# Kernel tuning notes

Measured on AMD Instinct MI355X. Metric: run time of the kernel, lower is better.

Reference implementation:

```python
import jax, jax.numpy as jnp
import numpy as np

B, D_BYTES, R, S, NSEG, OUT_DIM = 8, 128, 4096, 32768, 1024, 512
D_BITS = 8 * D_BYTES  # 1024


def setup_inputs() -> dict:
    key = jax.random.key(0)
    ks = jax.random.split(key, 9)
    u8 = lambda k, shape: jax.random.randint(k, shape, 0, 256, dtype=jnp.int32).astype(jnp.uint8)
    Q = u8(ks[0], (B, D_BYTES))
    Q_ok = u8(ks[1], (B, D_BYTES))
    refs = u8(ks[2], (R, D_BYTES))
    ok_pos = u8(ks[3], (R, D_BYTES))
    ref2seg = jax.random.randint(ks[4], (S,), 0, R, dtype=jnp.int32)
    segments = jnp.sort(jax.random.randint(ks[5], (S,), 0, NSEG, dtype=jnp.int32))
    W_o = jax.random.normal(ks[6], (D_BITS, OUT_DIM), dtype=jnp.float32) * (1.0 / np.sqrt(D_BITS))
    b_o = jnp.zeros((OUT_DIM,), dtype=jnp.float32)
    return {"Q": Q, "Q_ok": Q_ok, "refs": refs, "ok_pos": ok_pos,
            "ref2seg": ref2seg, "segments": segments, "N": NSEG,
            "W_o": W_o, "b_o": b_o}


def reference(Q, Q_ok, refs, ok_pos, ref2seg, segments, N, W_o, b_o):
    # values: unpack packed reference bit-sequences once: (R, d_bits) uint8
    values = jnp.unpackbits(refs, axis=1)

    def per_query(q, q_ok):
        # popcount sequence similarity, normalized by non-gap overlap length
        ok = jnp.sum(jax.lax.population_count(jnp.bitwise_and(q_ok, ok_pos)), axis=1)      # (R,)
        match = jnp.sum(jax.lax.population_count(jnp.bitwise_and(q, refs)), axis=1)        # (R,)
        dists = match / ok                                                                  # (R,) float32
        # numerically-stable segment softmax over ragged neighborhoods
        applied = jnp.take(dists, ref2seg)                                                  # (S,)
        mx = jnp.take(jax.ops.segment_max(applied, segments, num_segments=N), segments)
        e = applied - mx
        norm = jnp.take(jnp.log(jax.ops.segment_sum(jnp.exp(e), segments, num_segments=N)), segments)
        scores = jnp.exp(e - norm)                                                          # (S,)
        # gather values along edges, weight, scatter-sum into segments
        av = jnp.take(values, ref2seg, axis=0) * scores[:, None]                            # (S, d_bits)
        return jax.ops.segment_sum(av, segments, num_segments=N)                            # (N, d_bits)

    V = jax.vmap(per_query)(Q, Q_ok)        # (B, N, d_bits)
    return V @ W_o + b_o                     # (B, N, out_dim)
```

## Files before the change

kernel.cpp:

```cpp
#include <hip/hip_runtime.h>

#define B_Q   8
#define DB    128
#define R_REF 4096
#define S_EDGE 32768
#define NSEG  1024
#define DBITS 1024
#define OUTD  512

#define NB_WCONV 128
#define NB_UNPACK 2048
#define NB_DIST 8192
#define TILE_E 256

typedef __bf16 bf16_t;
typedef bf16_t bf16x8 __attribute__((ext_vector_type(8)));
typedef float  f32x4  __attribute__((ext_vector_type(4)));
typedef unsigned int u32;

__device__ inline unsigned short f2bf(float f){
  unsigned int u = __builtin_bit_cast(unsigned int, f);
  u = (u + 0x7fffu + ((u >> 16) & 1u)) >> 16;
  return (unsigned short)u;
}

__device__ __forceinline__ void gl_lds16(const unsigned short* g, unsigned short* l){
  __builtin_amdgcn_global_load_lds((const __attribute__((address_space(1))) u32*)g,
                                   (__attribute__((address_space(3))) u32*)l, 16, 0, 0);
}

__global__ __launch_bounds__(256) void k_prep(const float* __restrict__ W,
                                              unsigned short* __restrict__ WT,
                                              const int* __restrict__ refs,
                                              unsigned short* __restrict__ Rb,
                                              const int* __restrict__ Q,
                                              const int* __restrict__ Qok,
                                              const int* __restrict__ okpos,
                                              float* __restrict__ distsT){
  __shared__ float tile[64][65];
  const int bid = blockIdx.x;
  const int tid = threadIdx.x;

  if (bid < NB_WCONV){
    const int k0 = (bid & 15) * 64, o0 = (bid >> 4) * 64;
    const int tr = tid >> 6, tc = tid & 63;
    #pragma unroll
    for (int i = 0; i < 16; ++i)
      tile[tr + i*4][tc] = W[(size_t)(k0 + tr + i*4) * OUTD + o0 + tc];
    __syncthreads();
    #pragma unroll
    for (int i = 0; i < 16; ++i)
      WT[(size_t)(o0 + tr + i*4) * DBITS + k0 + tc] = f2bf(tile[tc][tr + i*4]);
  } else if (bid < NB_WCONV + NB_UNPACK){
    int t = (bid - NB_WCONV) * 256 + tid;
    int row = t >> 7, byte = t & 127;
    u32 v = (u32)refs[row * DB + byte];
    uint4 o;
    u32* w = (u32*)&o;
    #pragma unroll
    for (int i2 = 0; i2 < 4; ++i2){
      u32 b0 = (v >> (7 - 2*i2)) & 1u;
      u32 b1 = (v >> (6 - 2*i2)) & 1u;
      w[i2] = b0 * 0x3F80u | ((b1 * 0x3F80u) << 16);
    }
    *(uint4*)(Rb + (size_t)row * DBITS + byte * 8) = o;
  } else {
    int pair = (bid - NB_WCONV - NB_UNPACK) * 4 + (tid >> 6);
    int l = tid & 63;
    int b = pair >> 12;
    int r = pair & 4095;
    int q0 = Q[b*DB + l],    q1 = Q[b*DB + 64 + l];
    int a0 = Qok[b*DB + l],  a1 = Qok[b*DB + 64 + l];
    int f0 = refs[r*DB + l], f1 = refs[r*DB + 64 + l];
    int p0 = okpos[r*DB + l],p1 = okpos[r*DB + 64 + l];
    int m = __popc(q0 & f0) + __popc(q1 & f1);
    int o = __popc(a0 & p0) + __popc(a1 & p1);
    int v = m | (o << 16);
    #pragma unroll
    for (int off = 32; off; off >>= 1) v += __shfl_down(v, off);
    if (l == 0) distsT[r * 8 + b] = (float)(v & 0xffff) / (float)(v >> 16);
  }
}

__global__ __launch_bounds__(256) void k_ugemm(const unsigned short* __restrict__ Rb,
                                               const unsigned short* __restrict__ WT,
                                               unsigned short* __restrict__ U){
  __shared__ unsigned short As[2][64 * 128];
  __shared__ unsigned short Bs[2][64 * 128];
  const int tid = threadIdx.x;
  const int w = tid >> 6, l = tid & 63;
  const int tm = blockIdx.x * 64, tn = blockIdx.y * 64;
  const int wm = (w & 1) * 32, wn = (w >> 1) * 32;
  const int lr = l & 15, kq = l >> 4;

  f32x4 acc[2][2] = {};
  int cur = 0;

  #define STAGE(buf, K0)                                                                   \
    do {                                                                                   \
      _Pragma("unroll")                                                                    \
      for (int c = 0; c < 4; ++c){                                                         \
        int idx = c * 256 + tid;                                                           \
        int row = idx >> 4, ch = idx & 15;                                                 \
        int gch = ch ^ (row & 15);                                                         \
        gl_lds16(Rb + (size_t)(tm + row) * DBITS + (K0) + gch*8,                           \
                 As[buf] + row*128 + ch*8);                                                \
        gl_lds16(WT + (size_t)(tn + row) * DBITS + (K0) + gch*8,                           \
                 Bs[buf] + row*128 + ch*8);                                                \
      }                                                                                    \
    } while (0)

  STAGE(0, 0);
  __syncthreads();

  for (int s = 0; s < 8; ++s){
    if (s < 7) STAGE(cur ^ 1, (s + 1) * 128);
    #pragma unroll
    for (int kk = 0; kk < 4; ++kk){
      bf16x8 af[2], bfr[2];
      #pragma unroll
      for (int m = 0; m < 2; ++m){
        int row = wm + m*16 + lr;
        int ch  = (kk*4 + kq) ^ (row & 15);
        af[m] = __builtin_bit_cast(bf16x8, *(const uint4*)(As[cur] + row*128 + ch*8));
      }
      #pragma unroll
      for (int n = 0; n < 2; ++n){
        int row = wn + n*16 + lr;
        int ch  = (kk*4 + kq) ^ (row & 15);
        bfr[n] = __builtin_bit_cast(bf16x8, *(const uint4*)(Bs[cur] + row*128 + ch*8));
      }
      #pragma unroll
      for (int m = 0; m < 2; ++m)
        #pragma unroll
        for (int n = 0; n < 2; ++n)
          acc[m][n] = __builtin_amdgcn_mfma_f32_16x16x32_bf16(af[m], bfr[n], acc[m][n], 0, 0, 0);
    }
    __syncthreads();
    cur ^= 1;
  }
  #undef STAGE

  #pragma unroll
  for (int n = 0; n < 2; ++n)
    #pragma unroll
    for (int m = 0; m < 2; ++m){
      int row = tm + wm + m*16 + kq*4;
      int col = tn + wn + n*16 + lr;
      #pragma unroll
      for (int q = 0; q < 4; ++q)
        U[(size_t)(row + q) * OUTD + col] = f2bf(acc[m][n][q]);
    }
}

__global__ __launch_bounds__(256) void k_scat(const float* __restrict__ distsT,
                                              const int* __restrict__ ref2seg,
                                              const int* __restrict__ segments,
                                              const unsigned short* __restrict__ U,
                                              const float* __restrict__ bo,
                                              float* __restrict__ out){
  __shared__ float mbs[8], ibs[8];
  __shared__ float scl[TILE_E * 8];
  __shared__ int   rix[TILE_E];
  const int n = blockIdx.x;
  const int t = threadIdx.x;
  const int l = t & 63;

  int tgt = n + (l & 1);
  int lo = 0, hi = S_EDGE;
  #pragma unroll 1
  while (lo < hi){ int mid = (lo + hi) >> 1; if (segments[mid] < tgt) lo = mid + 1; else hi = mid; }
  const int start = __shfl(lo, 0);
  const int end   = __shfl(lo, 1);

  const float b0c = bo[2*t], b1c = bo[2*t + 1];
  float* op = out + (size_t)n * OUTD + 2*t;

  if (start >= end){
    #pragma unroll
    for (int j = 0; j < 8; ++j){ op[(size_t)j * NSEG * OUTD] = b0c; op[(size_t)j * NSEG * OUTD + 1] = b1c; }
    return;
  }

  if (t < 64){
    const int sb = t >> 3, es = t & 7;
    float m = -1e30f, s = 0.f;
    for (int e = start + es; e < end; e += 8){
      float d = distsT[ref2seg[e] * 8 + sb];
      float mn = fmaxf(m, d);
      s = s * __expf(m - mn) + __expf(d - mn);
      m = mn;
    }
    #pragma unroll
    for (int msk = 1; msk < 8; msk <<= 1){
      float mo = __shfl_xor(m, msk), so = __shfl_xor(s, msk);
      float mn = fmaxf(m, mo);
      s = s * __expf(m - mn) + so * __expf(mo - mn);
      m = mn;
    }
    if (es == 0){ mbs[sb] = m; ibs[sb] = 1.0f / s; }
  }
  __syncthreads();

  float acc[8][2];
  #pragma unroll
  for (int j = 0; j < 8; ++j){ acc[j][0] = 0.f; acc[j][1] = 0.f; }

  for (int e0 = start; e0 < end; e0 += TILE_E){
    const int cnt = min(TILE_E, end - e0);
    for (int i = t; i < cnt * 8; i += 256){
      int e = e0 + (i >> 3), b = i & 7;
      int r = ref2seg[e];
      if (b == 0) rix[i >> 3] = r;
      scl[i] = __expf(distsT[r*8 + b] - mbs[b]) * ibs[b];
    }
    __syncthreads();

    #pragma unroll 4
    for (int e = 0; e < cnt; ++e){
      int r = rix[e];
      float4 s0 = *(const float4*)(scl + e*8);
      float4 s1 = *(const float4*)(scl + e*8 + 4);
      u32 uu = *(const u32*)(U + ((size_t)r << 9) + 2*t);
      float ux = __builtin_bit_cast(float, uu << 16);
      float uy = __builtin_bit_cast(float, uu & 0xffff0000u);
      float ss[8] = {s0.x, s0.y, s0.z, s0.w, s1.x, s1.y, s1.z, s1.w};
      #pragma unroll
      for (int j = 0; j < 8; ++j){
        acc[j][0] += ss[j] * ux;
        acc[j][1] += ss[j] * uy;
      }
    }
    __syncthreads();
  }

  #pragma unroll
  for (int j = 0; j < 8; ++j){
    op[(size_t)j * NSEG * OUTD]     = acc[j][0] + b0c;
    op[(size_t)j * NSEG * OUTD + 1] = acc[j][1] + b1c;
  }
}

extern "C" void kernel_launch(void* const* d_in, const int* in_sizes, int n_in,
                              void* d_out, int out_size, void* d_ws, size_t ws_size,
                              hipStream_t stream) {
  const int*   Q        = (const int*)d_in[0];
  const int*   Qok      = (const int*)d_in[1];
  const int*   refs     = (const int*)d_in[2];
  const int*   okpos    = (const int*)d_in[3];
  const int*   ref2seg  = (const int*)d_in[4];
  const int*   segments = (const int*)d_in[5];
  const float* W        = (const float*)d_in[7];
  const float* bo       = (const float*)d_in[8];
  float* out = (float*)d_out;

  char* ws = (char*)d_ws;
  unsigned short* WT     = (unsigned short*)ws;
  float*          distsT = (float*)(ws + (1u<<20));
  unsigned short* Rb     = (unsigned short*)(ws + (2u<<20));
  unsigned short* U      = (unsigned short*)(ws + (11u<<20));

  k_prep <<<NB_WCONV + NB_UNPACK + NB_DIST, 256, 0, stream>>>(W, WT, refs, Rb, Q, Qok, okpos, distsT);
  k_ugemm<<<dim3(R_REF/64, OUTD/64), 256, 0, stream>>>(Rb, WT, U);
  k_scat <<<NSEG, 256, 0, stream>>>(distsT, ref2seg, segments, U, bo, out);
}
```

Baseline: 43.19 us.

## Merge three kernels into one cooperative persistent kernel with grid syncs

Replaces the three separate launches (prep, GEMM, scatter) with a single cooperative kernel of 512 persistent blocks. Prep and scatter work are grid-strided, and the phases are separated by grid.sync(). The GEMM tile mapping is swizzled by block index. The aim is to remove per-launch overhead and inter-kernel gaps. In exchange it adds grid-wide barrier cost, a 64KB static LDS footprint that limits blocks per CU, and lower parallelism in the prep phase.

```diff
diff --git a/kernel.cpp b/kernel.cpp
--- a/kernel.cpp
+++ b/kernel.cpp
@@ -1,4 +1,7 @@
 #include <hip/hip_runtime.h>
+#include <hip/hip_cooperative_groups.h>
+
+namespace cg = cooperative_groups;
 
 #define B_Q   8
 #define DB    128
@@ -11,6 +14,8 @@
 #define NB_WCONV 128
 #define NB_UNPACK 2048
 #define NB_DIST 8192
+#define NB_TOTAL (NB_WCONV + NB_UNPACK + NB_DIST)
+#define GRID 512
 #define TILE_E 256
 
 typedef __bf16 bf16_t;
@@ -29,215 +34,227 @@
                                    (__attribute__((address_space(3))) u32*)l, 16, 0, 0);
 }
 
-__global__ __launch_bounds__(256) void k_prep(const float* __restrict__ W,
-                                              unsigned short* __restrict__ WT,
-                                              const int* __restrict__ refs,
-                                              unsigned short* __restrict__ Rb,
-                                              const int* __restrict__ Q,
-                                              const int* __restrict__ Qok,
-                                              const int* __restrict__ okpos,
-                                              float* __restrict__ distsT){
-  __shared__ float tile[64][65];
-  const int bid = blockIdx.x;
+__global__ __launch_bounds__(256, 2) void k_all(const float* __restrict__ W,
+                                                unsigned short* __restrict__ WT,
+                                                const int* __restrict__ refs,
+                                                unsigned short* __restrict__ Rb,
+                                                const int* __restrict__ Q,
+                                                const int* __restrict__ Qok,
+                                                const int* __restrict__ okpos,
+                                                float* __restrict__ distsT,
+                                                const int* __restrict__ ref2seg,
+                                                const int* __restrict__ segments,
+                                                unsigned short* __restrict__ U,
+                                                const float* __restrict__ bo,
+                                                float* __restrict__ out){
+  __shared__ __align__(16) unsigned char SMRAW[65536];
   const int tid = threadIdx.x;
-
-  if (bid < NB_WCONV){
-    const int k0 = (bid & 15) * 64, o0 = (bid >> 4) * 64;
-    const int tr = tid >> 6, tc = tid & 63;
-    #pragma unroll
-    for (int i = 0; i < 16; ++i)
-      tile[tr + i*4][tc] = W[(size_t)(k0 + tr + i*4) * OUTD + o0 + tc];
-    __syncthreads();
-    #pragma unroll
-    for (int i = 0; i < 16; ++i)
-      WT[(size_t)(o0 + tr + i*4) * DBITS + k0 + tc] = f2bf(tile[tc][tr + i*4]);
-  } else if (bid < NB_WCONV + NB_UNPACK){
-    int t = (bid - NB_WCONV) * 256 + tid;
-    int row = t >> 7, byte = t & 127;
-    u32 v = (u32)refs[row * DB + byte];
-    uint4 o;
-    u32* w = (u32*)&o;
-    #pragma unroll
-    for (int i2 = 0; i2 < 4; ++i2){
-      u32 b0 = (v >> (7 - 2*i2)) & 1u;
-      u32 b1 = (v >> (6 - 2*i2)) & 1u;
-      w[i2] = b0 * 0x3F80u | ((b1 * 0x3F80u) << 16);
-    }
-    *(uint4*)(Rb + (size_t)row * DBITS + byte * 8) = o;
-  } else {
-    int pair = (bid - NB_WCONV - NB_UNPACK) * 4 + (tid >> 6);
-    int l = tid & 63;
-    int b = pair >> 12;
-    int r = pair & 4095;
-    int q0 = Q[b*DB + l],    q1 = Q[b*DB + 64 + l];
-    int a0 = Qok[b*DB + l],  a1 = Qok[b*DB + 64 + l];
-    int f0 = refs[r*DB + l], f1 = refs[r*DB + 64 + l];
-    int p0 = okpos[r*DB + l],p1 = okpos[r*DB + 64 + l];
-    int m = __popc(q0 & f0) + __popc(q1 & f1);
-    int o = __popc(a0 & p0) + __popc(a1 & p1);
-    int v = m | (o << 16);
-    #pragma unroll
-    for (int off = 32; off; off >>= 1) v += __shfl_down(v, off);
-    if (l == 0) distsT[r * 8 + b] = (float)(v & 0xffff) / (float)(v >> 16);
-  }
-}
-
-__global__ __launch_bounds__(256) void k_ugemm(const unsigned short* __restrict__ Rb,
-                                               const unsigned short* __restrict__ WT,
-                                               unsigned short* __restrict__ U){
-  __shared__ unsigned short As[2][64 * 128];
-  __shared__ unsigned short Bs[2][64 * 128];
-  const int tid = threadIdx.x;
-  const int w = tid >> 6, l = tid & 63;
-  const int tm = blockIdx.x * 64, tn = blockIdx.y * 64;
-  const int wm = (w & 1) * 32, wn = (w >> 1) * 32;
-  const int lr = l & 15, kq = l >> 4;
-
-  f32x4 acc[2][2] = {};
-  int cur = 0;
-
-  #define STAGE(buf, K0)                                                                   \
-    do {                                                                                   \
-      _Pragma("unroll")                                                                    \
-      for (int c = 0; c < 4; ++c){                                                         \
-        int idx = c * 256 + tid;                                                           \
-        int row = idx >> 4, ch = idx & 15;                                                 \
-        int gch = ch ^ (row & 15);                                                         \
-        gl_lds16(Rb + (size_t)(tm + row) * DBITS + (K0) + gch*8,                           \
-                 As[buf] + row*128 + ch*8);                                                \
-        gl_lds16(WT + (size_t)(tn + row) * DBITS + (K0) + gch*8,                           \
-                 Bs[buf] + row*128 + ch*8);                                                \
-      }                                                                                    \
-    } while (0)
-
-  STAGE(0, 0);
-  __syncthreads();
-
-  for (int s = 0; s < 8; ++s){
-    if (s < 7) STAGE(cur ^ 1, (s + 1) * 128);
-    #pragma unroll
-    for (int kk = 0; kk < 4; ++kk){
-      bf16x8 af[2], bfr[2];
-      #pragma unroll
-      for (int m = 0; m < 2; ++m){
-        int row = wm + m*16 + lr;
-        int ch  = (kk*4 + kq) ^ (row & 15);
-        af[m] = __builtin_bit_cast(bf16x8, *(const uint4*)(As[cur] + row*128 + ch*8));
-      }
-      #pragma unroll
-      for (int n = 0; n < 2; ++n){
-        int row = wn + n*16 + lr;
-        int ch  = (kk*4 + kq) ^ (row & 15);
-        bfr[n] = __builtin_bit_cast(bf16x8, *(const uint4*)(Bs[cur] + row*128 + ch*8));
-      }
-      #pragma unroll
-      for (int m = 0; m < 2; ++m)
-        #pragma unroll
-        for (int n = 0; n < 2; ++n)
-          acc[m][n] = __builtin_amdgcn_mfma_f32_16x16x32_bf16(af[m], bfr[n], acc[m][n], 0, 0, 0);
-    }
-    __syncthreads();
-    cur ^= 1;
-  }
-  #undef STAGE
-
-  #pragma unroll
-  for (int n = 0; n < 2; ++n)
-    #pragma unroll
-    for (int m = 0; m < 2; ++m){
-      int row = tm + wm + m*16 + kq*4;
-      int col = tn + wn + n*16 + lr;
-      #pragma unroll
-      for (int q = 0; q < 4; ++q)
-        U[(size_t)(row + q) * OUTD + col] = f2bf(acc[m][n][q]);
-    }
-}
-
-__global__ __launch_bounds__(256) void k_scat(const float* __restrict__ distsT,
-                                              const int* __restrict__ ref2seg,
-                                              const int* __restrict__ segments,
-                                              const unsigned short* __restrict__ U,
-                                              const float* __restrict__ bo,
-                                              float* __restrict__ out){
-  __shared__ float mbs[8], ibs[8];
-  __shared__ float scl[TILE_E * 8];
-  __shared__ int   rix[TILE_E];
-  const int n = blockIdx.x;
-  const int t = threadIdx.x;
-  const int l = t & 63;
-
-  int tgt = n + (l & 1);
-  int lo = 0, hi = S_EDGE;
-  #pragma unroll 1
-  while (lo < hi){ int mid = (lo + hi) >> 1; if (segments[mid] < tgt) lo = mid + 1; else hi = mid; }
-  const int start = __shfl(lo, 0);
-  const int end   = __shfl(lo, 1);
-
-  const float b0c = bo[2*t], b1c = bo[2*t + 1];
-  float* op = out + (size_t)n * OUTD + 2*t;
-
-  if (start >= end){
-    #pragma unroll
-    for (int j = 0; j < 8; ++j){ op[(size_t)j * NSEG * OUTD] = b0c; op[(size_t)j * NSEG * OUTD + 1] = b1c; }
-    return;
-  }
-
-  if (t < 64){
-    const int sb = t >> 3, es = t & 7;
-    float m = -1e30f, s = 0.f;
-    for (int e = start + es; e < end; e += 8){
-      float d = distsT[ref2seg[e] * 8 + sb];
-      float mn = fmaxf(m, d);
-      s = s * __expf(m - mn) + __expf(d - mn);
-      m = mn;
-    }
-    #pragma unroll
-    for (int msk = 1; msk < 8; msk <<= 1){
-      float mo = __shfl_xor(m, msk), so = __shfl_xor(s, msk);
-      float mn = fmaxf(m, mo);
-      s = s * __expf(m - mn) + so * __expf(mo - mn);
-      m = mn;
-    }
-    if (es == 0){ mbs[sb] = m; ibs[sb] = 1.0f / s; }
-  }
-  __syncthreads();
-
-  float acc[8][2];
-  #pragma unroll
-  for (int j = 0; j < 8; ++j){ acc[j][0] = 0.f; acc[j][1] = 0.f; }
-
-  for (int e0 = start; e0 < end; e0 += TILE_E){
-    const int cnt = min(TILE_E, end - e0);
-    for (int i = t; i < cnt * 8; i += 256){
-      int e = e0 + (i >> 3), b = i & 7;
-      int r = ref2seg[e];
-      if (b == 0) rix[i >> 3] = r;
-      scl[i] = __expf(distsT[r*8 + b] - mbs[b]) * ibs[b];
-    }
-    __syncthreads();
-
-    #pragma unroll 4
-    for (int e = 0; e < cnt; ++e){
-      int r = rix[e];
-      float4 s0 = *(const float4*)(scl + e*8);
-      float4 s1 = *(const float4*)(scl + e*8 + 4);
-      u32 uu = *(const u32*)(U + ((size_t)r << 9) + 2*t);
-      float ux = __builtin_bit_cast(float, uu << 16);
-      float uy = __builtin_bit_cast(float, uu & 0xffff0000u);
-      float ss[8] = {s0.x, s0.y, s0.z, s0.w, s1.x, s1.y, s1.z, s1.w};
-      #pragma unroll
-      for (int j = 0; j < 8; ++j){
-        acc[j][0] += ss[j] * ux;
-        acc[j][1] += ss[j] * uy;
-      }
+  cg::grid_group grid = cg::this_grid();
+
+  for (int vb = blockIdx.x; vb < NB_TOTAL; vb += GRID){
+    if (vb < NB_WCONV){
+      float (*tile)[65] = (float(*)[65])SMRAW;
+      const int k0 = (vb & 15) * 64, o0 = (vb >> 4) * 64;
+      const int tr = tid >> 6, tc = tid & 63;
+      #pragma unroll
+      for (int i = 0; i < 16; ++i)
+        tile[tr + i*4][tc] = W[(size_t)(k0 + tr + i*4) * OUTD + o0 + tc];
+      __syncthreads();
+      #pragma unroll
+      for (int i = 0; i < 16; ++i)
+        WT[(size_t)(o0 + tr + i*4) * DBITS + k0 + tc] = f2bf(tile[tc][tr + i*4]);
+    } else if (vb < NB_WCONV + NB_UNPACK){
+      int t = (vb - NB_WCONV) * 256 + tid;
+      int row = t >> 7, byte = t & 127;
+      u32 v = (u32)refs[row * DB + byte];
+      uint4 o;
+      u32* w = (u32*)&o;
+      #pragma unroll
+      for (int i2 = 0; i2 < 4; ++i2){
+        u32 b0 = (v >> (7 - 2*i2)) & 1u;
+        u32 b1 = (v >> (6 - 2*i2)) & 1u;
+        w[i2] = b0 * 0x3F80u | ((b1 * 0x3F80u) << 16);
+      }
+      *(uint4*)(Rb + (size_t)row * DBITS + byte * 8) = o;
+    } else {
+      int pair = (vb - NB_WCONV - NB_UNPACK) * 4 + (tid >> 6);
+      int l = tid & 63;
+      int b = pair >> 12;
+      int r = pair & 4095;
+      int q0 = Q[b*DB + l],    q1 = Q[b*DB + 64 + l];
+      int a0 = Qok[b*DB + l],  a1 = Qok[b*DB + 64 + l];
+      int f0 = refs[r*DB + l], f1 = refs[r*DB + 64 + l];
+      int p0 = okpos[r*DB + l],p1 = okpos[r*DB + 64 + l];
+      int m = __popc(q0 & f0) + __popc(q1 & f1);
+      int o = __popc(a0 & p0) + __popc(a1 & p1);
+      int v = m | (o << 16);
+      #pragma unroll
+      for (int off = 32; off; off >>= 1) v += __shfl_down(v, off);
+      if (l == 0) distsT[r * 8 + b] = (float)(v & 0xffff) / (float)(v >> 16);
     }
     __syncthreads();
   }
 
-  #pragma unroll
-  for (int j = 0; j < 8; ++j){
-    op[(size_t)j * NSEG * OUTD]     = acc[j][0] + b0c;
-    op[(size_t)j * NSEG * OUTD + 1] = acc[j][1] + b1c;
+  grid.sync();
+
+  {
+    unsigned short* AS = (unsigned short*)SMRAW;
+    unsigned short* BS = (unsigned short*)(SMRAW + 32768);
+    const int bid = blockIdx.x;
+    const int virt = ((bid & 7) << 6) | (bid >> 3);
+    const int tm = (virt >> 3) * 64, tn = (virt & 7) * 64;
+    const int w = tid >> 6, l = tid & 63;
+    const int wm = (w & 1) * 32, wn = (w >> 1) * 32;
+    const int lr = l & 15, kq = l >> 4;
+
+    f32x4 acc[2][2] = {};
+    int cur = 0;
+
+    #define STAGE(buf, K0)                                                                 \
+      do {                                                                                 \
+        _Pragma("unroll")                                                                  \
+        for (int c = 0; c < 4; ++c){                                                       \
+          int idx = c * 256 + tid;                                                         \
+          int row = idx >> 4, ch = idx & 15;                                               \
+          int gch = ch ^ (row & 15);                                                       \
+          gl_lds16(Rb + (size_t)(tm + row) * DBITS + (K0) + gch*8,                         \
+                   AS + (buf)*8192 + row*128 + ch*8);                                      \
+          gl_lds16(WT + (size_t)(tn + row) * DBITS + (K0) + gch*8,                         \
+                   BS + (buf)*8192 + row*128 + ch*8);                                      \
+        }                                                                                  \
+      } while (0)
+
+    STAGE(0, 0);
+    __syncthreads();
+
+    for (int s = 0; s < 8; ++s){
+      if (s < 7) STAGE(cur ^ 1, (s + 1) * 128);
+      #pragma unroll
+      for (int kk = 0; kk < 4; ++kk){
+        bf16x8 af[2], bfr[2];
+        #pragma unroll
+        for (int m = 0; m < 2; ++m){
+          int row = wm + m*16 + lr;
+          int ch  = (kk*4 + kq) ^ (row & 15);
+          af[m] = __builtin_bit_cast(bf16x8, *(const uint4*)(AS + cur*8192 + row*128 + ch*8));
+        }
+        #pragma unroll
+        for (int n = 0; n < 2; ++n){
+          int row = wn + n*16 + lr;
+          int ch  = (kk*4 + kq) ^ (row & 15);
+          bfr[n] = __builtin_bit_cast(bf16x8, *(const uint4*)(BS + cur*8192 + row*128 + ch*8));
+        }
+        #pragma unroll
+        for (int m = 0; m < 2; ++m)
+          #pragma unroll
+          for (int n = 0; n < 2; ++n)
+            acc[m][n] = __builtin_amdgcn_mfma_f32_16x16x32_bf16(af[m], bfr[n], acc[m][n], 0, 0, 0);
+      }
+      __syncthreads();
+      cur ^= 1;
+    }
+    #undef STAGE
+
+    #pragma unroll
+    for (int n = 0; n < 2; ++n)
+      #pragma unroll
+      for (int m = 0; m < 2; ++m){
+        int row = tm + wm + m*16 + kq*4;
+        int col = tn + wn + n*16 + lr;
+        #pragma unroll
+        for (int q = 0; q < 4; ++q)
+          U[(size_t)(row + q) * OUTD + col] = f2bf(acc[m][n][q]);
+      }
+  }
+
+  grid.sync();
+
+  {
+    float* mbs = (float*)SMRAW;
+    float* ibs = (float*)SMRAW + 8;
+    int*   rix = (int*)((float*)SMRAW + 16);
+    float* scl = (float*)(SMRAW + 4096);
+    const int t = threadIdx.x;
+    const int l = t & 63;
+    const float b0c = bo[2*t], b1c = bo[2*t + 1];
+
+    for (int n = blockIdx.x; n < NSEG; n += GRID){
+      int tgt = n + (l & 1);
+      int lo = 0, hi = S_EDGE;
+      #pragma unroll 1
+      while (lo < hi){ int mid = (lo + hi) >> 1; if (segments[mid] < tgt) lo = mid + 1; else hi = mid; }
+      const int start = __shfl(lo, 0);
+      const int end   = __shfl(lo, 1);
+
+      float* op = out + (size_t)n * OUTD + 2*t;
+
+      if (start >= end){
+        #pragma unroll
+        for (int j = 0; j < 8; ++j){
+          op[(size_t)j * NSEG * OUTD]     = b0c;
+          op[(size_t)j * NSEG * OUTD + 1] = b1c;
+        }
+        continue;
+      }
+
+      if (t < 64){
+        const int sb = t >> 3, es = t & 7;
+        float m = -1e30f, s = 0.f;
+        for (int e = start + es; e < end; e += 8){
+          float d = distsT[ref2seg[e] * 8 + sb];
+          float mn = fmaxf(m, d);
+          s = s * __expf(m - mn) + __expf(d - mn);
+          m = mn;
+        }
+        #pragma unroll
+        for (int msk = 1; msk < 8; msk <<= 1){
+          float mo = __shfl_xor(m, msk), so = __shfl_xor(s, msk);
+          float mn = fmaxf(m, mo);
+          s = s * __expf(m - mn) + so * __expf(mo - mn);
+          m = mn;
+        }
+        if (es == 0){ mbs[sb] = m; ibs[sb] = 1.0f / s; }
+      }
+      __syncthreads();
+
+      float acc[8][2];
+      #pragma unroll
+      for (int j = 0; j < 8; ++j){ acc[j][0] = 0.f; acc[j][1] = 0.f; }
+
+      for (int e0 = start; e0 < end; e0 += TILE_E){
+        const int cnt = min(TILE_E, end - e0);
+        for (int i = t; i < cnt * 8; i += 256){
+          int e = e0 + (i >> 3), b = i & 7;
+          int r = ref2seg[e];
+          if (b == 0) rix[i >> 3] = r;
+          scl[i] = __expf(distsT[r*8 + b] - mbs[b]) * ibs[b];
+        }
+        __syncthreads();
+
+        #pragma unroll 4
+        for (int e = 0; e < cnt; ++e){
+          int r = rix[e];
+          float4 s0 = *(const float4*)(scl + e*8);
+          float4 s1 = *(const float4*)(scl + e*8 + 4);
+          u32 uu = *(const u32*)(U + ((size_t)r << 9) + 2*t);
+          float ux = __builtin_bit_cast(float, uu << 16);
+          float uy = __builtin_bit_cast(float, uu & 0xffff0000u);
+          float ss[8] = {s0.x, s0.y, s0.z, s0.w, s1.x, s1.y, s1.z, s1.w};
+          #pragma unroll
+          for (int j = 0; j < 8; ++j){
+            acc[j][0] += ss[j] * ux;
+            acc[j][1] += ss[j] * uy;
+          }
+        }
+        __syncthreads();
+      }
+
+      #pragma unroll
+      for (int j = 0; j < 8; ++j){
+        op[(size_t)j * NSEG * OUTD]     = acc[j][0] + b0c;
+        op[(size_t)j * NSEG * OUTD + 1] = acc[j][1] + b1c;
+      }
+    }
   }
 }
 
@@ -260,7 +277,8 @@
   unsigned short* Rb     = (unsigned short*)(ws + (2u<<20));
   unsigned short* U      = (unsigned short*)(ws + (11u<<20));
 
-  k_prep <<<NB_WCONV + NB_UNPACK + NB_DIST, 256, 0, stream>>>(W, WT, refs, Rb, Q, Qok, okpos, distsT);
-  k_ugemm<<<dim3(R_REF/64, OUTD/64), 256, 0, stream>>>(Rb, WT, U);
-  k_scat <<<NSEG, 256, 0, stream>>>(distsT, ref2seg, segments, U, bo, out);
-}
+  void* args[] = {(void*)&W, (void*)&WT, (void*)&refs, (void*)&Rb, (void*)&Q, (void*)&Qok,
+                  (void*)&okpos, (void*)&distsT, (void*)&ref2seg, (void*)&segments,
+                  (void*)&U, (void*)&bo, (void*)&out};
+  hipLaunchCooperativeKernel((void*)k_all, dim3(GRID), dim3(256), args, 0, stream);
+}
```

Result: slower. 172.2 us (+298.7%).

## Fuse bit unpacking into GEMM A-staging and precompute segment bounds in prep

Applied to the files above, without the earlier changes.

Removes the separate unpack stage that wrote an 8 MB bf16 expansion of refs. The GEMM now loads packed bytes directly and expands them into swizzled LDS for the A tile, while the B tile keeps async global-to-LDS loads. Segment start offsets are computed once by binary search in the prep kernel, so the scatter kernel reads two ints per segment instead of searching per block. This cuts memory traffic, but the A staging now goes through registers and ALU work inside the GEMM pipeline.

```diff
diff --git a/kernel.cpp b/kernel.cpp
--- a/kernel.cpp
+++ b/kernel.cpp
@@ -9,8 +9,8 @@
 #define OUTD  512
 
 #define NB_WCONV 128
-#define NB_UNPACK 2048
 #define NB_DIST 8192
+#define NB_BOUNDS 4
 #define TILE_E 256
 
 typedef __bf16 bf16_t;
@@ -32,11 +32,12 @@
 __global__ __launch_bounds__(256) void k_prep(const float* __restrict__ W,
                                               unsigned short* __restrict__ WT,
                                               const int* __restrict__ refs,
-                                              unsigned short* __restrict__ Rb,
                                               const int* __restrict__ Q,
                                               const int* __restrict__ Qok,
                                               const int* __restrict__ okpos,
-                                              float* __restrict__ distsT){
+                                              float* __restrict__ distsT,
+                                              const int* __restrict__ segments,
+                                              int* __restrict__ segstart){
   __shared__ float tile[64][65];
   const int bid = blockIdx.x;
   const int tid = threadIdx.x;
@@ -51,21 +52,8 @@
     #pragma unroll
     for (int i = 0; i < 16; ++i)
       WT[(size_t)(o0 + tr + i*4) * DBITS + k0 + tc] = f2bf(tile[tc][tr + i*4]);
-  } else if (bid < NB_WCONV + NB_UNPACK){
-    int t = (bid - NB_WCONV) * 256 + tid;
-    int row = t >> 7, byte = t & 127;
-    u32 v = (u32)refs[row * DB + byte];
-    uint4 o;
-    u32* w = (u32*)&o;
-    #pragma unroll
-    for (int i2 = 0; i2 < 4; ++i2){
-      u32 b0 = (v >> (7 - 2*i2)) & 1u;
-      u32 b1 = (v >> (6 - 2*i2)) & 1u;
-      w[i2] = b0 * 0x3F80u | ((b1 * 0x3F80u) << 16);
-    }
-    *(uint4*)(Rb + (size_t)row * DBITS + byte * 8) = o;
-  } else {
-    int pair = (bid - NB_WCONV - NB_UNPACK) * 4 + (tid >> 6);
+  } else if (bid < NB_WCONV + NB_DIST){
+    int pair = (bid - NB_WCONV) * 4 + (tid >> 6);
     int l = tid & 63;
     int b = pair >> 12;
     int r = pair & 4095;
@@ -79,14 +67,21 @@
     #pragma unroll
     for (int off = 32; off; off >>= 1) v += __shfl_down(v, off);
     if (l == 0) distsT[r * 8 + b] = (float)(v & 0xffff) / (float)(v >> 16);
-  }
-}
-
-__global__ __launch_bounds__(256) void k_ugemm(const unsigned short* __restrict__ Rb,
+  } else {
+    int n = (bid - NB_WCONV - NB_DIST) * 256 + tid;
+    int lo = 0, hi = S_EDGE;
+    #pragma unroll 1
+    while (lo < hi){ int mid = (lo + hi) >> 1; if (segments[mid] < n) lo = mid + 1; else hi = mid; }
+    segstart[n] = lo;
+    if (n == 0) segstart[NSEG] = S_EDGE;
+  }
+}
+
+__global__ __launch_bounds__(256) void k_ugemm(const int* __restrict__ refs,
                                                const unsigned short* __restrict__ WT,
                                                unsigned short* __restrict__ U){
-  __shared__ unsigned short As[2][64 * 128];
-  __shared__ unsigned short Bs[2][64 * 128];
+  __shared__ unsigned short AS[2 * 64 * 128];
+  __shared__ unsigned short BS[2 * 64 * 128];
   const int tid = threadIdx.x;
   const int w = tid >> 6, l = tid & 63;
   const int tm = blockIdx.x * 64, tn = blockIdx.y * 64;
@@ -96,25 +91,46 @@
   f32x4 acc[2][2] = {};
   int cur = 0;
 
-  #define STAGE(buf, K0)                                                                   \
+  #define STAGE_B(buf, K0)                                                                 \
     do {                                                                                   \
       _Pragma("unroll")                                                                    \
       for (int c = 0; c < 4; ++c){                                                         \
         int idx = c * 256 + tid;                                                           \
         int row = idx >> 4, ch = idx & 15;                                                 \
         int gch = ch ^ (row & 15);                                                         \
-        gl_lds16(Rb + (size_t)(tm + row) * DBITS + (K0) + gch*8,                           \
-                 As[buf] + row*128 + ch*8);                                                \
         gl_lds16(WT + (size_t)(tn + row) * DBITS + (K0) + gch*8,                           \
-                 Bs[buf] + row*128 + ch*8);                                                \
+                 BS + (buf)*8192 + row*128 + ch*8);                                        \
       }                                                                                    \
     } while (0)
 
-  STAGE(0, 0);
+  #define STAGE_A(buf, K0)                                                                 \
+    do {                                                                                   \
+      int row = tid >> 2, j0 = (tid & 3) * 4;                                              \
+      int4 rv = *(const int4*)(refs + (size_t)(tm + row) * DB + (K0)/8 + j0);              \
+      const int rx = row & 15;                                                             \
+      int vv[4] = {rv.x, rv.y, rv.z, rv.w};                                                \
+      _Pragma("unroll")                                                                    \
+      for (int j = 0; j < 4; ++j){                                                         \
+        u32 v = (u32)vv[j];                                                                \
+        uint4 o;                                                                           \
+        u32* wp = (u32*)&o;                                                                \
+        _Pragma("unroll")                                                                  \
+        for (int i2 = 0; i2 < 4; ++i2){                                                    \
+          u32 b0 = (v >> (7 - 2*i2)) & 1u;                                                 \
+          u32 b1 = (v >> (6 - 2*i2)) & 1u;                                                 \
+          wp[i2] = b0 * 0x3F80u | ((b1 * 0x3F80u) << 16);                                  \
+        }                                                                                  \
+        int lch = (j0 + j) ^ rx;                                                           \
+        *(uint4*)(AS + (buf)*8192 + row*128 + lch*8) = o;                                  \
+      }                                                                                    \
+    } while (0)
+
+  STAGE_B(0, 0);
+  STAGE_A(0, 0);
   __syncthreads();
 
   for (int s = 0; s < 8; ++s){
-    if (s < 7) STAGE(cur ^ 1, (s + 1) * 128);
+    if (s < 7){ STAGE_B(cur ^ 1, (s + 1) * 128); STAGE_A(cur ^ 1, (s + 1) * 128); }
     #pragma unroll
     for (int kk = 0; kk < 4; ++kk){
       bf16x8 af[2], bfr[2];
@@ -122,13 +138,13 @@
       for (int m = 0; m < 2; ++m){
         int row = wm + m*16 + lr;
         int ch  = (kk*4 + kq) ^ (row & 15);
-        af[m] = __builtin_bit_cast(bf16x8, *(const uint4*)(As[cur] + row*128 + ch*8));
+        af[m] = __builtin_bit_cast(bf16x8, *(const uint4*)(AS + cur*8192 + row*128 + ch*8));
       }
       #pragma unroll
       for (int n = 0; n < 2; ++n){
         int row = wn + n*16 + lr;
         int ch  = (kk*4 + kq) ^ (row & 15);
-        bfr[n] = __builtin_bit_cast(bf16x8, *(const uint4*)(Bs[cur] + row*128 + ch*8));
+        bfr[n] = __builtin_bit_cast(bf16x8, *(const uint4*)(BS + cur*8192 + row*128 + ch*8));
       }
       #pragma unroll
       for (int m = 0; m < 2; ++m)
@@ -139,7 +155,8 @@
     __syncthreads();
     cur ^= 1;
   }
-  #undef STAGE
+  #undef STAGE_A
+  #undef STAGE_B
 
   #pragma unroll
   for (int n = 0; n < 2; ++n)
@@ -155,7 +172,7 @@
 
 __global__ __launch_bounds__(256) void k_scat(const float* __restrict__ distsT,
                                               const int* __restrict__ ref2seg,
-                                              const int* __restrict__ segments,
+                                              const int* __restrict__ segstart,
                                               const unsigned short* __restrict__ U,
                                               const float* __restrict__ bo,
                                               float* __restrict__ out){
@@ -164,21 +181,18 @@
   __shared__ int   rix[TILE_E];
   const int n = blockIdx.x;
   const int t = threadIdx.x;
-  const int l = t & 63;
-
-  int tgt = n + (l & 1);
-  int lo = 0, hi = S_EDGE;
-  #pragma unroll 1
-  while (lo < hi){ int mid = (lo + hi) >> 1; if (segments[mid] < tgt) lo = mid + 1; else hi = mid; }
-  const int start = __shfl(lo, 0);
-  const int end   = __shfl(lo, 1);
+
+  const int start = segstart[n], end = segstart[n + 1];
 
   const float b0c = bo[2*t], b1c = bo[2*t + 1];
   float* op = out + (size_t)n * OUTD + 2*t;
 
   if (start >= end){
     #pragma unroll
-    for (int j = 0; j < 8; ++j){ op[(size_t)j * NSEG * OUTD] = b0c; op[(size_t)j * NSEG * OUTD + 1] = b1c; }
+    for (int j = 0; j < 8; ++j){
+      op[(size_t)j * NSEG * OUTD]     = b0c;
+      op[(size_t)j * NSEG * OUTD + 1] = b1c;
+    }
     return;
   }
 
@@ -255,12 +269,13 @@
   float* out = (float*)d_out;
 
   char* ws = (char*)d_ws;
-  unsigned short* WT     = (unsigned short*)ws;
-  float*          distsT = (float*)(ws + (1u<<20));
-  unsigned short* Rb     = (unsigned short*)(ws + (2u<<20));
-  unsigned short* U      = (unsigned short*)(ws + (11u<<20));
-
-  k_prep <<<NB_WCONV + NB_UNPACK + NB_DIST, 256, 0, stream>>>(W, WT, refs, Rb, Q, Qok, okpos, distsT);
-  k_ugemm<<<dim3(R_REF/64, OUTD/64), 256, 0, stream>>>(Rb, WT, U);
-  k_scat <<<NSEG, 256, 0, stream>>>(distsT, ref2seg, segments, U, bo, out);
-}
+  unsigned short* WT       = (unsigned short*)ws;
+  float*          distsT   = (float*)(ws + (1u<<20));
+  int*            segstart = (int*)(ws + (1u<<20) + (160u<<10));
+  unsigned short* U        = (unsigned short*)(ws + (11u<<20));
+
+  k_prep <<<NB_WCONV + NB_DIST + NB_BOUNDS, 256, 0, stream>>>(W, WT, refs, Q, Qok, okpos,
+                                                              distsT, segments, segstart);
+  k_ugemm<<<dim3(R_REF/64, OUTD/64), 256, 0, stream>>>(refs, WT, U);
+  k_scat <<<NSEG, 256, 0, stream>>>(distsT, ref2seg, segstart, U, bo, out);
+}
```

Result: no change. 43.43 us (+0.6%).
